# Kernel tuning notes

Hardware: AMD Instinct MI355X
Metric: run time of the kernel (lower is better)

Reference implementation:

```python
import jax, jax.numpy as jnp
import numpy as np

N_NODES = 100_000
N_EDGES = 800_000
NODE_DIM = 192
CONF_DIM = 64
HID = 256  # graphsage_in == graphsage_hidden
ALPHA = 0.2  # LeakyReLU negative slope


def _lrelu(x):
    return jnp.where(x >= 0, x, ALPHA * x)


def _sage_max(x, src, dst, wl, bl, wr):
    # PyG SAGEConv, aggr='max': out = lin_l(max_{j in N(i)} x_j) + lin_r(x_i)
    msgs = x[src]                                   # [E, HID] gather
    agg = jax.ops.segment_max(msgs, dst, num_segments=N_NODES)  # [N, HID]
    agg = jnp.where(jnp.isneginf(agg), 0.0, agg)    # isolated nodes -> 0
    return agg @ wl + bl + x @ wr


def _mlp2(x, w0, b0, w1, b1):
    # Linear -> LeakyReLU(0.2) -> Linear (activation only between layers)
    return _lrelu(x @ w0 + b0) @ w1 + b1


def setup_inputs() -> dict:
    key = jax.random.key(0)
    ks = jax.random.split(key, 16)
    s = 0.05
    inp = {
        "node_features": jax.random.normal(ks[0], (N_NODES, NODE_DIM), jnp.float32),
        "config_features": jax.random.normal(ks[1], (N_NODES, CONF_DIM), jnp.float32),
        "edges": jax.random.randint(ks[2], (2, N_EDGES), 0, N_NODES, jnp.int32),
        "prenet_w0": jax.random.normal(ks[3], (HID, NODE_DIM), jnp.float32) * s,
        "prenet_b0": jnp.zeros((NODE_DIM,), jnp.float32),
        "prenet_w1": jax.random.normal(ks[4], (NODE_DIM, NODE_DIM), jnp.float32) * s,
        "prenet_b1": jnp.zeros((NODE_DIM,), jnp.float32),
    }
    for l, k0 in ((0, 5), (1, 10)):
        inp[f"sage{l}_wl"] = jax.random.normal(ks[k0], (HID, HID), jnp.float32) * s
        inp[f"sage{l}_bl"] = jnp.zeros((HID,), jnp.float32)
        inp[f"sage{l}_wr"] = jax.random.normal(ks[k0 + 1], (HID, HID), jnp.float32) * s
        inp[f"mlp{l}_w0"] = jax.random.normal(ks[k0 + 2], (HID, NODE_DIM), jnp.float32) * s
        inp[f"mlp{l}_b0"] = jnp.zeros((NODE_DIM,), jnp.float32)
        inp[f"mlp{l}_w1"] = jax.random.normal(ks[k0 + 3], (NODE_DIM, NODE_DIM), jnp.float32) * s
        inp[f"mlp{l}_b1"] = jnp.zeros((NODE_DIM,), jnp.float32)
    return inp


def reference(node_features, config_features, edges,
              prenet_w0, prenet_b0, prenet_w1, prenet_b1,
              sage0_wl, sage0_bl, sage0_wr, mlp0_w0, mlp0_b0, mlp0_w1, mlp0_b1,
              sage1_wl, sage1_bl, sage1_wr, mlp1_w0, mlp1_b0, mlp1_w1, mlp1_b1):
    src, dst = edges[0], edges[1]
    x = jnp.concatenate([config_features, node_features], axis=1)  # [N, 256]
    x = _lrelu(_mlp2(x, prenet_w0, prenet_b0, prenet_w1, prenet_b1))  # [N, 192]
    layers = [
        (sage0_wl, sage0_bl, sage0_wr, mlp0_w0, mlp0_b0, mlp0_w1, mlp0_b1),
        (sage1_wl, sage1_bl, sage1_wr, mlp1_w0, mlp1_b0, mlp1_w1, mlp1_b1),
    ]
    for swl, sbl, swr, mw0, mb0, mw1, mb1 in layers:
        y = jnp.concatenate([config_features, x], axis=1)          # [N, 256]
        y = _sage_max(y, src, dst, swl, sbl, swr)                  # [N, 256]
        y = _lrelu(_mlp2(y, mw0, mb0, mw1, mb1))                   # [N, 192]
        x = x + y
    return x
```

## Files before the change

### kernel.cpp

```cpp
#include <hip/hip_runtime.h>
#include <stdint.h>

#define N_NODES 100000
#define N_EDGES 800000

typedef unsigned short u16;
typedef __attribute__((ext_vector_type(8))) short bf16x8;
typedef __attribute__((ext_vector_type(8))) unsigned short ushort8;
typedef __attribute__((ext_vector_type(4))) float f32x4;
typedef __attribute__((ext_vector_type(4))) int i32x4;
typedef __attribute__((ext_vector_type(4))) unsigned int u32x4;

struct alignas(8) U16x4 { u16 x, y, z, w; };

__device__ __forceinline__ u16 f2b(float f) {
    union { float f; unsigned u; } x; x.f = f;
    unsigned r = (x.u + 0x7FFFu + ((x.u >> 16) & 1u)) >> 16;
    return (u16)r;
}
__device__ __forceinline__ float b2f(u16 h) {
    union { unsigned u; float f; } x; x.u = ((unsigned)h) << 16;
    return x.f;
}
__device__ __forceinline__ u16 keyb(u16 h) {
    u16 m = (u16)((short)h >> 15);
    return (u16)(h ^ (0x8000u | (m & 0x7FFFu)));
}
__device__ __forceinline__ u16 unkey(u16 k) {
    u16 m = (u16)((short)k >> 15);
    return (u16)(k ^ (0x8000u | (~m & 0x7FFFu)));
}
__device__ __forceinline__ unsigned pkmax(unsigned a, unsigned b) {
    unsigned d;
    asm("v_pk_max_u16 %0, %1, %2" : "=v"(d) : "v"(a), "v"(b));
    return d;
}
__device__ __forceinline__ u32x4 pkmax4(u32x4 a, u32x4 b) {
    u32x4 r;
    r.x = pkmax(a.x, b.x); r.y = pkmax(a.y, b.y);
    r.z = pkmax(a.z, b.z); r.w = pkmax(a.w, b.w);
    return r;
}

__device__ __forceinline__ void gload_lds16(const void* g, void* l) {
    __builtin_amdgcn_global_load_lds(
        (const __attribute__((address_space(1))) char*)(uintptr_t)g,
        (__attribute__((address_space(3))) char*)(uintptr_t)l,
        16, 0, 0);
}

__device__ __forceinline__ int simgG(int row, int col) { return row * 136 + col; }
__device__ __forceinline__ int simgF(int row, int col) { return row * 200 + col; }


struct PackSeg { const float* a; const float* b; u16* dst; int K0, K1, Ncol, beg, end; };
struct PackArgs { PackSeg s[8]; };


__global__ void k_prep(const float* __restrict__ conf, const float* __restrict__ node,
                       u16* __restrict__ conf16, u16* __restrict__ node16,
                       u16* __restrict__ keyed, int* __restrict__ deg,
                       PackArgs p, int packTotal) {
    const int c4 = N_NODES * 64 / 4;
    const int n4 = N_NODES * 192 / 4;
    int i = blockIdx.x * blockDim.x + threadIdx.x;
    if (i < c4) {
        float4 v = ((const float4*)conf)[i];
        U16x4 o; o.x = f2b(v.x); o.y = f2b(v.y); o.z = f2b(v.z); o.w = f2b(v.w);
        ((U16x4*)conf16)[i] = o;
        U16x4 ko; ko.x = keyb(o.x); ko.y = keyb(o.y); ko.z = keyb(o.z); ko.w = keyb(o.w);
        int n = i >> 4;
        ((U16x4*)keyed)[n * 64 + (i & 15)] = ko;
    } else if (i < c4 + n4) {
        float4 v = ((const float4*)node)[i - c4];
        U16x4 o; o.x = f2b(v.x); o.y = f2b(v.y); o.z = f2b(v.z); o.w = f2b(v.w);
        ((U16x4*)node16)[i - c4] = o;
    } else if (i < c4 + n4 + N_NODES / 4) {
        i32x4 z = {0, 0, 0, 0};
        ((i32x4*)deg)[i - c4 - n4] = z;
    } else {
        int idx = i - (c4 + n4 + N_NODES / 4);
        if (idx < packTotal) {
            #pragma unroll
            for (int si = 0; si < 8; ++si) {
                if (idx >= p.s[si].beg && idx < p.s[si].end) {
                    int li = idx - p.s[si].beg;
                    int Ncol = p.s[si].Ncol, K0 = p.s[si].K0;
                    int kq = li & 7;
                    int t = li >> 3;
                    int c15 = t & 15; t >>= 4;
                    int k8 = t & 3;  t >>= 2;
                    int nb = Ncol >> 4;
                    int cb = t % nb;
                    int ks = t / nb;
                    int col = cb * 16 + c15;
                    int k = ks * 32 + k8 * 8 + kq;
                    float v = (k < K0) ? p.s[si].a[(size_t)k * Ncol + col]
                                       : p.s[si].b[(size_t)(k - K0) * Ncol + col];
                    p.s[si].dst[li] = f2b(v);
                }
            }
        }
    }
}


__global__ void k_count(const int* __restrict__ dst, int* __restrict__ deg) {
    int e = blockIdx.x * blockDim.x + threadIdx.x;
    if (e < N_EDGES) atomicAdd(&deg[dst[e]], 1);
}

__global__ void k_scan1(const int* __restrict__ deg, int* __restrict__ excl,
                        int* __restrict__ bsum, int n) {
    __shared__ int sh[512];
    int t = threadIdx.x;
    int base = blockIdx.x * 2048 + t * 4;
    int v0 = (base + 0 < n) ? deg[base + 0] : 0;
    int v1 = (base + 1 < n) ? deg[base + 1] : 0;
    int v2 = (base + 2 < n) ? deg[base + 2] : 0;
    int v3 = (base + 3 < n) ? deg[base + 3] : 0;
    int tot = v0 + v1 + v2 + v3;
    sh[t] = tot;
    __syncthreads();
    for (int off = 1; off < 512; off <<= 1) {
        int x = (t >= off) ? sh[t - off] : 0;
        __syncthreads();
        sh[t] += x;
        __syncthreads();
    }
    int run = sh[t] - tot;
    if (base + 0 < n) excl[base + 0] = run; run += v0;
    if (base + 1 < n) excl[base + 1] = run; run += v1;
    if (base + 2 < n) excl[base + 2] = run; run += v2;
    if (base + 3 < n) excl[base + 3] = run;
    if (t == 511) bsum[blockIdx.x] = sh[t];
}

__global__ void k_scan2(int* __restrict__ bsum, int nb) {
    __shared__ int sh[64];
    int t = threadIdx.x;
    int v = (t < nb) ? bsum[t] : 0;
    sh[t] = v;
    __syncthreads();
    for (int off = 1; off < 64; off <<= 1) {
        int x = (t >= off) ? sh[t - off] : 0;
        __syncthreads();
        sh[t] += x;
        __syncthreads();
    }
    if (t < nb) bsum[t] = sh[t] - v;
}

__global__ void k_scan3(int* __restrict__ excl, const int* __restrict__ bsum,
                        int* __restrict__ cursor, int n) {
    int i = blockIdx.x * blockDim.x + threadIdx.x;
    if (i < n) {
        int v = excl[i] + bsum[i >> 11];
        excl[i] = v;
        cursor[i] = v;
    }
}

__global__ void k_scatter(const int* __restrict__ src, const int* __restrict__ dst,
                          int* __restrict__ cursor, int* __restrict__ esrc) {
    int e = blockIdx.x * blockDim.x + threadIdx.x;
    if (e < N_EDGES) {
        int p = atomicAdd(&cursor[dst[e]], 1);
        esrc[p] = src[e];
    }
}


template<int CHUNKS>
__global__ __launch_bounds__(256) void k_agg(
    const u16* __restrict__ keyed,
    const int* __restrict__ indptr, const int* __restrict__ deg,
    const int* __restrict__ iend, const int* __restrict__ esrc,
    u16* __restrict__ agg, u16* __restrict__ aggC, int nquads) {
    __shared__ int se[512];
    __shared__ int sinfo[2];
    const int lane = threadIdx.x & 63;
    constexpr int ACTIVE = (CHUNKS == 32) ? 64 : 48;
    const int e_sub = (CHUNKS == 32) ? (lane >> 5) : (lane >= 24 ? 1 : 0);
    int ch = lane - e_sub * CHUNKS;
    if (ch < 0 || ch >= CHUNKS) ch = 0;
    const u16* bp = keyed + ((CHUNKS == 32) ? 0 : 64) + ch * 8;

    for (int q = blockIdx.x; q < nquads; q += gridDim.x) {
        const int b4 = q * 4;
        if (threadIdx.x == 0) {
            sinfo[0] = indptr[b4];
            sinfo[1] = iend[b4 + 3];
        }
        __syncthreads();
        const int sbase = sinfo[0];
        const int slen = sinfo[1] - sbase;
        const bool useLds = slen <= 512;
        if (useLds) {
            for (int i = threadIdx.x; i < slen; i += 256) se[i] = esrc[sbase + i];
        }
        __syncthreads();

        const int node = b4 + (threadIdx.x >> 6);
        const int start = indptr[node];
        const int d = deg[node];

        u32x4 m = {0u, 0u, 0u, 0u};

        if (lane < ACTIVE && d > 0) {
            const int rounds = (d + 15) >> 4;
            const int lbase = start - sbase;
            const int dm1 = d - 1;
            for (int rr = 0; rr < rounds; ++rr) {
                const int b0 = rr * 16 + e_sub;
                int s[8];
                if (useLds) {
                    #pragma unroll
                    for (int t = 0; t < 8; ++t) s[t] = se[lbase + min(b0 + 2 * t, dm1)];
                } else {
                    #pragma unroll
                    for (int t = 0; t < 8; ++t) s[t] = esrc[start + min(b0 + 2 * t, dm1)];
                }
                u32x4 v0 = *(const u32x4*)(bp + (size_t)s[0] * 256);
                u32x4 v1 = *(const u32x4*)(bp + (size_t)s[1] * 256);
                u32x4 v2 = *(const u32x4*)(bp + (size_t)s[2] * 256);
                u32x4 v3 = *(const u32x4*)(bp + (size_t)s[3] * 256);
                u32x4 v4 = *(const u32x4*)(bp + (size_t)s[4] * 256);
                u32x4 v5 = *(const u32x4*)(bp + (size_t)s[5] * 256);
                u32x4 v6 = *(const u32x4*)(bp + (size_t)s[6] * 256);
                u32x4 v7 = *(const u32x4*)(bp + (size_t)s[7] * 256);
                u32x4 a = pkmax4(pkmax4(v0, v1), pkmax4(v2, v3));
                u32x4 b = pkmax4(pkmax4(v4, v5), pkmax4(v6, v7));
                m = pkmax4(m, pkmax4(a, b));
            }
        }

        if (CHUNKS == 32) {
            m.x = pkmax(m.x, __shfl_xor(m.x, 32, 64));
            m.y = pkmax(m.y, __shfl_xor(m.y, 32, 64));
            m.z = pkmax(m.z, __shfl_xor(m.z, 32, 64));
            m.w = pkmax(m.w, __shfl_xor(m.w, 32, 64));
        } else {
            m.x = pkmax(m.x, __shfl(m.x, lane + 24, 64));
            m.y = pkmax(m.y, __shfl(m.y, lane + 24, 64));
            m.z = pkmax(m.z, __shfl(m.z, lane + 24, 64));
            m.w = pkmax(m.w, __shfl(m.w, lane + 24, 64));
        }

        unsigned wv[4] = {m.x, m.y, m.z, m.w};
        ushort8 o;
        #pragma unroll
        for (int j = 0; j < 4; ++j) {
            u16 klo = (u16)(wv[j] & 0xFFFFu), khi = (u16)(wv[j] >> 16);
            o[2 * j]     = (d > 0) ? unkey(klo) : (u16)0;
            o[2 * j + 1] = (d > 0) ? unkey(khi) : (u16)0;
        }

        if (CHUNKS == 32) {
            if (lane < 32) {
                *(ushort8*)(agg + (size_t)node * 256 + lane * 8) = o;
                if (lane < 8)
                    *(ushort8*)(aggC + (size_t)node * 64 + lane * 8) = o;
            }
        } else {
            if (lane < 24)
                *(ushort8*)(agg + (size_t)node * 256 + 64 + lane * 8) = o;
        }
        __syncthreads();
    }
}


struct SegA { const u16* p; int K; int stride; };

template<int BN>
__global__ __launch_bounds__(512) void k_gemm(
    SegA s0, SegA s1, SegA s2, SegA s3,
    const u16* __restrict__ Bt,
    const float* __restrict__ bias,
    u16* __restrict__ outb,
    int nrows)
{
    constexpr int FN = BN / 64;
    constexpr int ASZ = 128 * 32;
    __shared__ u16 lds[2][ASZ + BN * 32] __attribute__((aligned(16)));

    const int tid = threadIdx.x;
    const int wave = tid >> 6;
    const int lane = tid & 63;
    const int wr = wave >> 2;
    const int wc = wave & 3;
    const int rowbase = blockIdx.x * 128;
    const u16* segp[4] = {s0.p, s1.p, s2.p, s3.p};
    const int segK[4]  = {s0.K, s1.K, s2.K, s3.K};
    const int segS[4]  = {s0.stride, s1.stride, s2.stride, s3.stride};
    const int nk = (segK[0] + segK[1] + segK[2] + segK[3]) >> 5;

    const int arow = ((tid >> 6) << 4) | (tid & 15);
    int grow = rowbase + arow; if (grow >= nrows) grow = nrows - 1;
    const int ak8 = (tid >> 4) & 3;
    int seg = 0;
    const u16* gA = segp[0] + (size_t)grow * segS[0] + ak8 * 8;
    int segleft = segK[0] >> 5;
    const u16* gB0 = Bt + (size_t)tid * 8;
    const u16* gB1 = Bt + (size_t)(512 + tid) * 8;
    const int wb = wave * 512;

    auto adv = [&]() {
        gA += 32;
        if (--segleft == 0) {
            while (seg < 3) {
                ++seg;
                if (segK[seg] > 0) {
                    gA = segp[seg] + (size_t)grow * segS[seg] + ak8 * 8;
                    segleft = segK[seg] >> 5;
                    break;
                }
            }
        }
        gB0 += BN * 32;
        gB1 += BN * 32;
    };
    auto stage = [&](int buf) {
        gload_lds16(gA, &lds[buf][wb]);
        gload_lds16(gB0, &lds[buf][ASZ + wb]);
        if constexpr (BN == 256) {
            gload_lds16(gB1, &lds[buf][ASZ + 4096 + wb]);
        } else {
            if (tid < 256) gload_lds16(gB1, &lds[buf][ASZ + 4096 + wb]);
        }
    };

    f32x4 zero = {0.f, 0.f, 0.f, 0.f};
    f32x4 acc[4][FN];
    #pragma unroll
    for (int fm = 0; fm < 4; ++fm)
        #pragma unroll
        for (int fn = 0; fn < FN; ++fn)
            acc[fm][fn] = zero;

    stage(0); adv();
    __syncthreads();

    const int l15 = lane & 15, l4 = lane >> 4;

    for (int ks = 0; ks < nk; ++ks) {
        const int cur = ks & 1;
        if (ks + 1 < nk) { stage(cur ^ 1); adv(); }
        const u16* la = &lds[cur][0];
        const u16* lb = &lds[cur][ASZ];
        bf16x8 a[4], b[FN];
        #pragma unroll
        for (int fm = 0; fm < 4; ++fm)
            a[fm] = *(const bf16x8*)(la + (wr * 4 + fm) * 512 + lane * 8);
        #pragma unroll
        for (int fn = 0; fn < FN; ++fn)
            b[fn] = *(const bf16x8*)(lb + (wc * FN + fn) * 512 + lane * 8);
        #pragma unroll
        for (int fm = 0; fm < 4; ++fm)
            #pragma unroll
            for (int fn = 0; fn < FN; ++fn)
                acc[fm][fn] = __builtin_amdgcn_mfma_f32_16x16x32_bf16(a[fm], b[fn], acc[fm][fn], 0, 0, 0);
        __syncthreads();
    }

    u16* sbuf = &lds[0][0];
    #pragma unroll
    for (int chunk = 0; chunk < 2; ++chunk) {
        if ((wc >> 1) == chunk) {
            const int cbase = (wc & 1) * 64;
            #pragma unroll
            for (int fn = 0; fn < FN; ++fn) {
                const int cp = cbase + fn * 16 + l15;
                const float bs = bias[chunk * 128 + cp];
                #pragma unroll
                for (int fm = 0; fm < 4; ++fm) {
                    const int rbase = wr * 64 + fm * 16 + l4 * 4;
                    #pragma unroll
                    for (int r = 0; r < 4; ++r)
                        sbuf[simgG(rbase + r, cp)] = f2b(acc[fm][fn][r] + bs);
                }
            }
        }
        __syncthreads();
        #pragma unroll
        for (int j = 0; j < 4; ++j) {
            const int chk = j * 512 + tid;
            const int row = chk >> 4;
            const int cp = (chk & 15) * 8;
            const int gr = rowbase + row;
            if (gr < nrows) {
                ushort8 hv = *(const ushort8*)&sbuf[simgG(row, cp)];
                *(ushort8*)(outb + (size_t)gr * 256 + chunk * 128 + cp) = hv;
            }
        }
        __syncthreads();
    }
}


template<int EPI>
__global__ __launch_bounds__(512) void k_fused(
    const u16* __restrict__ A0, int K0,
    const u16* __restrict__ A1, int K1,
    const u16* __restrict__ B1t, const float* __restrict__ bias1,
    const u16* __restrict__ B2t, const float* __restrict__ bias2,
    float* __restrict__ outf, u16* __restrict__ outb,
    const u16* __restrict__ resid16, u16* __restrict__ keyed,
    int nrows)
{
    __shared__ u16 lds[25592] __attribute__((aligned(16)));

    const int tid = threadIdx.x;
    const int wave = tid >> 6;
    const int lane = tid & 63;
    const int wr = wave >> 2;
    const int wc = wave & 3;
    const int l15 = lane & 15, l4 = lane >> 4;
    const int rowbase = blockIdx.x * 128;
    const int nk1 = (K0 + K1) >> 5;

    const int arow = ((tid >> 6) << 4) | (tid & 15);
    int grow = rowbase + arow; if (grow >= nrows) grow = nrows - 1;
    const int ak8 = (tid >> 4) & 3;
    const u16* gA = A0 + (size_t)grow * K0 + ak8 * 8;
    int segleft = K0 >> 5;
    const u16* gB0 = B1t + (size_t)tid * 8;
    const u16* gB1 = B1t + (size_t)(512 + tid) * 8;
    const int wb = wave * 512;

    auto adv = [&]() {
        gA += 32;
        if (--segleft == 0 && K1 > 0) {
            gA = A1 + (size_t)grow * K1 + ak8 * 8;
            segleft = K1 >> 5;
        }
        gB0 += 6144;
        gB1 += 6144;
    };
    auto stage = [&](int buf) {
        gload_lds16(gA, &lds[buf * 4096 + wb]);
        gload_lds16(gB0, &lds[8192 + buf * 6144 + wb]);
        if (tid < 256) gload_lds16(gB1, &lds[8192 + buf * 6144 + 4096 + wb]);
    };

    f32x4 zero = {0.f, 0.f, 0.f, 0.f};
    f32x4 acc[4][3];
    #pragma unroll
    for (int fm = 0; fm < 4; ++fm)
        #pragma unroll
        for (int fn = 0; fn < 3; ++fn)
            acc[fm][fn] = zero;

    stage(0); adv();
    __syncthreads();

    for (int ks = 0; ks < nk1; ++ks) {
        const int cur = ks & 1;
        if (ks + 1 < nk1) { stage(cur ^ 1); adv(); }
        const u16* la = &lds[cur * 4096];
        const u16* lb = &lds[8192 + cur * 6144];
        bf16x8 a[4], b[3];
        #pragma unroll
        for (int fm = 0; fm < 4; ++fm)
            a[fm] = *(const bf16x8*)(la + (wr * 4 + fm) * 512 + lane * 8);
        #pragma unroll
        for (int fn = 0; fn < 3; ++fn)
            b[fn] = *(const bf16x8*)(lb + (wc * 3 + fn) * 512 + lane * 8);
        #pragma unroll
        for (int fm = 0; fm < 4; ++fm)
            #pragma unroll
            for (int fn = 0; fn < 3; ++fn)
                acc[fm][fn] = __builtin_amdgcn_mfma_f32_16x16x32_bf16(a[fm], b[fn], acc[fm][fn], 0, 0, 0);
        __syncthreads();
    }

    {
        const int c0 = wc * 48;
        #pragma unroll
        for (int fn = 0; fn < 3; ++fn) {
            const int c = c0 + fn * 16 + l15;
            const float bs = bias1[c];
            const int coff = (c >> 5) * 4096 + ((c >> 3) & 3) * 128 + (c & 7);
            #pragma unroll
            for (int fm = 0; fm < 4; ++fm) {
                const int rb = wr * 4 + fm;
                #pragma unroll
                for (int rr = 0; rr < 4; ++rr) {
                    const int r16 = l4 * 4 + rr;
                    float v = acc[fm][fn][rr] + bs;
                    v = (v >= 0.f) ? v : 0.2f * v;
                    lds[coff + rb * 512 + r16 * 8] = f2b(v);
                }
            }
        }
    }
    __syncthreads();

    bf16x8 breg[18];
    #pragma unroll
    for (int ks = 0; ks < 6; ++ks)
        #pragma unroll
        for (int fn = 0; fn < 3; ++fn)
            breg[ks * 3 + fn] = *(const bf16x8*)(B2t + (size_t)(ks * 12 + wc * 3 + fn) * 512 + lane * 8);

    f32x4 acc2[4][3];
    #pragma unroll
    for (int fm = 0; fm < 4; ++fm)
        #pragma unroll
        for (int fn = 0; fn < 3; ++fn)
            acc2[fm][fn] = zero;

    #pragma unroll
    for (int ks = 0; ks < 6; ++ks) {
        bf16x8 a2[4];
        #pragma unroll
        for (int fm = 0; fm < 4; ++fm)
            a2[fm] = *(const bf16x8*)(&lds[ks * 4096 + (wr * 4 + fm) * 512 + lane * 8]);
        #pragma unroll
        for (int fm = 0; fm < 4; ++fm)
            #pragma unroll
            for (int fn = 0; fn < 3; ++fn)
                acc2[fm][fn] = __builtin_amdgcn_mfma_f32_16x16x32_bf16(a2[fm], breg[ks * 3 + fn], acc2[fm][fn], 0, 0, 0);
    }
    __syncthreads();

    {
        const int c0 = wc * 48;
        #pragma unroll
        for (int fn = 0; fn < 3; ++fn) {
            const int c = c0 + fn * 16 + l15;
            const float bs = bias2[c];
            #pragma unroll
            for (int fm = 0; fm < 4; ++fm) {
                const int rbase = wr * 64 + fm * 16 + l4 * 4;
                #pragma unroll
                for (int r = 0; r < 4; ++r) {
                    float v = acc2[fm][fn][r] + bs;
                    v = (v >= 0.f) ? v : 0.2f * v;
                    lds[simgF(rbase + r, c)] = f2b(v);
                }
            }
        }
    }
    __syncthreads();

    #pragma unroll
    for (int j = 0; j < 6; ++j) {
        const int chk = j * 512 + tid;
        const int row = chk / 24;
        const int c = (chk - row * 24) * 8;
        const int gr = rowbase + row;
        if (gr < nrows) {
            ushort8 hv = *(const ushort8*)&lds[simgF(row, c)];
            if (EPI == 4) {
                ushort8 rv = *(const ushort8*)(resid16 + (size_t)gr * 192 + c);
                f32x4 o0, o1;
                #pragma unroll
                for (int k = 0; k < 4; ++k) {
                    o0[k] = b2f(hv[k]) + b2f(rv[k]);
                    o1[k] = b2f(hv[k + 4]) + b2f(rv[k + 4]);
                }
                *(f32x4*)(outf + (size_t)gr * 192 + c) = o0;
                *(f32x4*)(outf + (size_t)gr * 192 + c + 4) = o1;
            } else if (EPI == 5) {
                *(ushort8*)(outb + (size_t)gr * 192 + c) = hv;
                ushort8 kv;
                #pragma unroll
                for (int k = 0; k < 8; ++k) kv[k] = keyb(hv[k]);
                *(ushort8*)(keyed + (size_t)gr * 256 + 64 + c) = kv;
            } else {
                ushort8 rv = *(const ushort8*)(resid16 + (size_t)gr * 192 + c);
                ushort8 nb, kv;
                #pragma unroll
                for (int k = 0; k < 8; ++k) {
                    u16 hb = f2b(b2f(hv[k]) + b2f(rv[k]));
                    nb[k] = hb;
                    kv[k] = keyb(hb);
                }
                *(ushort8*)(outb + (size_t)gr * 192 + c) = nb;
                *(ushort8*)(keyed + (size_t)gr * 256 + 64 + c) = kv;
            }
        }
    }
}


extern "C" void kernel_launch(void* const* d_in, const int* in_sizes, int n_in,
                              void* d_out, int out_size, void* d_ws, size_t ws_size,
                              hipStream_t stream)
{
    (void)in_sizes; (void)n_in; (void)out_size; (void)ws_size;
    const float* node = (const float*)d_in[0];
    const float* conf = (const float*)d_in[1];
    const int* edges  = (const int*)d_in[2];
    const float* pw0  = (const float*)d_in[3];
    const float* pb0  = (const float*)d_in[4];
    const float* pw1  = (const float*)d_in[5];
    const float* pb1  = (const float*)d_in[6];
    const float* W[14];
    for (int i = 0; i < 14; ++i) W[i] = (const float*)d_in[7 + i];
    float* out = (float*)d_out;
    const int* e_src = edges;
    const int* e_dst = edges + N_EDGES;

    u16* keyed = (u16*)d_out;

    char* w = (char*)d_ws;
    auto alloc = [&](size_t b) { char* p = w; w += (b + 255) & ~(size_t)255; return p; };
    u16* conf16 = (u16*)alloc((size_t)N_NODES * 64 * 2);
    u16* node16 = (u16*)alloc((size_t)N_NODES * 192 * 2);
    u16* x16    = (u16*)alloc((size_t)N_NODES * 192 * 2);
    u16* agg16  = (u16*)alloc((size_t)N_NODES * 256 * 2);
    u16* aggC   = (u16*)alloc((size_t)N_NODES * 64 * 2);
    int* deg    = (int*)alloc((size_t)N_NODES * 4);
    int* indptr = (int*)alloc((size_t)N_NODES * 4);
    int* cursor = (int*)alloc((size_t)N_NODES * 4);
    int* esrc   = (int*)alloc((size_t)N_EDGES * 4);
    int* bsum   = (int*)alloc(4096);
    u16* pw0t   = (u16*)alloc((size_t)192 * 256 * 2);
    u16* pw1t   = (u16*)alloc((size_t)192 * 192 * 2);
    u16 *sB[2], *mw0t[2], *mw1t[2];
    for (int l = 0; l < 2; ++l) {
        sB[l]   = (u16*)alloc((size_t)256 * 512 * 2);
        mw0t[l] = (u16*)alloc((size_t)192 * 256 * 2);
        mw1t[l] = (u16*)alloc((size_t)192 * 192 * 2);
    }

    {
        PackArgs pa;
        int off = 0;
        auto seg = [&](int i, const float* a, int K0, const float* b, int K1, int Ncol, u16* dst) {
            int sz = Ncol * (K0 + K1);
            pa.s[i] = {a, b, dst, K0, K1, Ncol, off, off + sz};
            off += sz;
        };
        seg(0, pw0, 256, nullptr, 0, 192, pw0t);
        seg(1, pw1, 192, nullptr, 0, 192, pw1t);
        seg(2, W[0], 256, W[2], 256, 256, sB[0]);
        seg(3, W[3], 256, nullptr, 0, 192, mw0t[0]);
        seg(4, W[5], 192, nullptr, 0, 192, mw1t[0]);
        seg(5, W[7], 256, W[9], 256, 256, sB[1]);
        seg(6, W[10], 256, nullptr, 0, 192, mw0t[1]);
        seg(7, W[12], 192, nullptr, 0, 192, mw1t[1]);
        const int tot = N_NODES * 64 / 4 + N_NODES * 192 / 4 + N_NODES / 4 + off;
        k_prep<<<(tot + 255) / 256, 256, 0, stream>>>(conf, node, conf16, node16,
                                                      keyed, deg, pa, off);
    }
    k_count<<<(N_EDGES + 255) / 256, 256, 0, stream>>>(e_dst, deg);
    int nb = (N_NODES + 2047) / 2048;
    k_scan1<<<nb, 512, 0, stream>>>(deg, indptr, bsum, N_NODES);
    k_scan2<<<1, 64, 0, stream>>>(bsum, nb);
    k_scan3<<<(N_NODES + 255) / 256, 256, 0, stream>>>(indptr, bsum, cursor, N_NODES);
    k_scatter<<<(N_EDGES + 255) / 256, 256, 0, stream>>>(e_src, e_dst, cursor, esrc);

    const int gblk = (N_NODES + 127) / 128;
    const int nquads = N_NODES / 4;
    k_fused<5><<<gblk, 512, 0, stream>>>(conf16, 64, node16, 192,
                                         pw0t, pb0, pw1t, pb1,
                                         nullptr, x16, nullptr, keyed, N_NODES);
    for (int l = 0; l < 2; ++l) {
        if (l == 0) {
            k_agg<32><<<2048, 256, 0, stream>>>(keyed, indptr, deg, cursor, esrc,
                                                agg16, aggC, nquads);
            k_gemm<256><<<gblk, 512, 0, stream>>>(
                SegA{agg16, 256, 256}, SegA{conf16, 64, 64},
                SegA{x16, 192, 192}, SegA{nullptr, 0, 0},
                sB[0], W[1], agg16, N_NODES);
        } else {
            k_agg<24><<<2048, 256, 0, stream>>>(keyed, indptr, deg, cursor, esrc,
                                                agg16, aggC, nquads);
            k_gemm<256><<<gblk, 512, 0, stream>>>(
                SegA{aggC, 64, 64}, SegA{agg16 + 64, 192, 256},
                SegA{conf16, 64, 64}, SegA{x16, 192, 192},
                sB[1], W[8], agg16, N_NODES);
        }
        if (l == 0)
            k_fused<6><<<gblk, 512, 0, stream>>>(agg16, 256, nullptr, 0,
                                                 mw0t[0], W[4], mw1t[0], W[6],
                                                 nullptr, x16, x16, keyed, N_NODES);
        else
            k_fused<4><<<gblk, 512, 0, stream>>>(agg16, 256, nullptr, 0,
                                                 mw0t[1], W[11], mw1t[1], W[13],
                                                 out, nullptr, x16, nullptr, N_NODES);
    }
}
```

Baseline: 446.0 us.

## Split keyed gather buffer into dense conf and x arrays, one quad per block

The interleaved 256-wide keyed buffer is split into a 64-wide conf array and a 192-wide x array with dense strides. The layer-1 gather, which reads only the x part, now touches contiguous 384-byte rows instead of strided 512-byte rows, which improves cache-line use. The aggregation kernel also drops its grid-stride loop and launches one block per 4-node quad, removing the per-iteration barriers at the cost of more, shorter-lived blocks. keyedC is placed after keyedX inside the output buffer, which relies on that buffer being large enough.

```diff
diff --git a/kernel.cpp b/kernel.cpp
--- a/kernel.cpp
+++ b/kernel.cpp
@@ -59,7 +59,7 @@
 
 __global__ void k_prep(const float* __restrict__ conf, const float* __restrict__ node,
                        u16* __restrict__ conf16, u16* __restrict__ node16,
-                       u16* __restrict__ keyed, int* __restrict__ deg,
+                       u16* __restrict__ keyedC, int* __restrict__ deg,
                        PackArgs p, int packTotal) {
     const int c4 = N_NODES * 64 / 4;
     const int n4 = N_NODES * 192 / 4;
@@ -69,8 +69,7 @@
         U16x4 o; o.x = f2b(v.x); o.y = f2b(v.y); o.z = f2b(v.z); o.w = f2b(v.w);
         ((U16x4*)conf16)[i] = o;
         U16x4 ko; ko.x = keyb(o.x); ko.y = keyb(o.y); ko.z = keyb(o.z); ko.w = keyb(o.w);
-        int n = i >> 4;
-        ((U16x4*)keyed)[n * 64 + (i & 15)] = ko;
+        ((U16x4*)keyedC)[i] = ko;
     } else if (i < c4 + n4) {
         float4 v = ((const float4*)node)[i - c4];
         U16x4 o; o.x = f2b(v.x); o.y = f2b(v.y); o.z = f2b(v.z); o.w = f2b(v.w);
@@ -173,100 +172,106 @@
 
 template<int CHUNKS>
 __global__ __launch_bounds__(256) void k_agg(
-    const u16* __restrict__ keyed,
+    const u16* __restrict__ keyedC, const u16* __restrict__ keyedX,
     const int* __restrict__ indptr, const int* __restrict__ deg,
     const int* __restrict__ iend, const int* __restrict__ esrc,
-    u16* __restrict__ agg, u16* __restrict__ aggC, int nquads) {
+    u16* __restrict__ agg, u16* __restrict__ aggC) {
     __shared__ int se[512];
     __shared__ int sinfo[2];
+    const int b4 = blockIdx.x * 4;
+    if (threadIdx.x == 0) {
+        sinfo[0] = indptr[b4];
+        sinfo[1] = iend[b4 + 3];
+    }
+    __syncthreads();
+    const int sbase = sinfo[0];
+    const int slen = sinfo[1] - sbase;
+    const bool useLds = slen <= 512;
+    if (useLds) {
+        for (int i = threadIdx.x; i < slen; i += 256) se[i] = esrc[sbase + i];
+    }
+    __syncthreads();
+
+    const int node = b4 + (threadIdx.x >> 6);
     const int lane = threadIdx.x & 63;
     constexpr int ACTIVE = (CHUNKS == 32) ? 64 : 48;
     const int e_sub = (CHUNKS == 32) ? (lane >> 5) : (lane >= 24 ? 1 : 0);
     int ch = lane - e_sub * CHUNKS;
     if (ch < 0 || ch >= CHUNKS) ch = 0;
-    const u16* bp = keyed + ((CHUNKS == 32) ? 0 : 64) + ch * 8;
-
-    for (int q = blockIdx.x; q < nquads; q += gridDim.x) {
-        const int b4 = q * 4;
-        if (threadIdx.x == 0) {
-            sinfo[0] = indptr[b4];
-            sinfo[1] = iend[b4 + 3];
-        }
-        __syncthreads();
-        const int sbase = sinfo[0];
-        const int slen = sinfo[1] - sbase;
-        const bool useLds = slen <= 512;
-        if (useLds) {
-            for (int i = threadIdx.x; i < slen; i += 256) se[i] = esrc[sbase + i];
-        }
-        __syncthreads();
-
-        const int node = b4 + (threadIdx.x >> 6);
-        const int start = indptr[node];
-        const int d = deg[node];
-
-        u32x4 m = {0u, 0u, 0u, 0u};
-
-        if (lane < ACTIVE && d > 0) {
-            const int rounds = (d + 15) >> 4;
-            const int lbase = start - sbase;
-            const int dm1 = d - 1;
-            for (int rr = 0; rr < rounds; ++rr) {
-                const int b0 = rr * 16 + e_sub;
-                int s[8];
-                if (useLds) {
-                    #pragma unroll
-                    for (int t = 0; t < 8; ++t) s[t] = se[lbase + min(b0 + 2 * t, dm1)];
-                } else {
-                    #pragma unroll
-                    for (int t = 0; t < 8; ++t) s[t] = esrc[start + min(b0 + 2 * t, dm1)];
-                }
-                u32x4 v0 = *(const u32x4*)(bp + (size_t)s[0] * 256);
-                u32x4 v1 = *(const u32x4*)(bp + (size_t)s[1] * 256);
-                u32x4 v2 = *(const u32x4*)(bp + (size_t)s[2] * 256);
-                u32x4 v3 = *(const u32x4*)(bp + (size_t)s[3] * 256);
-                u32x4 v4 = *(const u32x4*)(bp + (size_t)s[4] * 256);
-                u32x4 v5 = *(const u32x4*)(bp + (size_t)s[5] * 256);
-                u32x4 v6 = *(const u32x4*)(bp + (size_t)s[6] * 256);
-                u32x4 v7 = *(const u32x4*)(bp + (size_t)s[7] * 256);
-                u32x4 a = pkmax4(pkmax4(v0, v1), pkmax4(v2, v3));
-                u32x4 b = pkmax4(pkmax4(v4, v5), pkmax4(v6, v7));
-                m = pkmax4(m, pkmax4(a, b));
-            }
-        }
-
-        if (CHUNKS == 32) {
-            m.x = pkmax(m.x, __shfl_xor(m.x, 32, 64));
-            m.y = pkmax(m.y, __shfl_xor(m.y, 32, 64));
-            m.z = pkmax(m.z, __shfl_xor(m.z, 32, 64));
-            m.w = pkmax(m.w, __shfl_xor(m.w, 32, 64));
-        } else {
-            m.x = pkmax(m.x, __shfl(m.x, lane + 24, 64));
-            m.y = pkmax(m.y, __shfl(m.y, lane + 24, 64));
-            m.z = pkmax(m.z, __shfl(m.z, lane + 24, 64));
-            m.w = pkmax(m.w, __shfl(m.w, lane + 24, 64));
-        }
-
-        unsigned wv[4] = {m.x, m.y, m.z, m.w};
-        ushort8 o;
-        #pragma unroll
-        for (int j = 0; j < 4; ++j) {
-            u16 klo = (u16)(wv[j] & 0xFFFFu), khi = (u16)(wv[j] >> 16);
-            o[2 * j]     = (d > 0) ? unkey(klo) : (u16)0;
-            o[2 * j + 1] = (d > 0) ? unkey(khi) : (u16)0;
-        }
-
-        if (CHUNKS == 32) {
-            if (lane < 32) {
-                *(ushort8*)(agg + (size_t)node * 256 + lane * 8) = o;
-                if (lane < 8)
-                    *(ushort8*)(aggC + (size_t)node * 64 + lane * 8) = o;
-            }
-        } else {
-            if (lane < 24)
-                *(ushort8*)(agg + (size_t)node * 256 + 64 + lane * 8) = o;
-        }
-        __syncthreads();
+    const int start = indptr[node];
+    const int d = deg[node];
+
+    const u16* bp;
+    int stride;
+    if (CHUNKS == 32) {
+        const bool isConf = ch < 8;
+        bp = isConf ? (keyedC + ch * 8) : (keyedX + (ch - 8) * 8);
+        stride = isConf ? 64 : 192;
+    } else {
+        bp = keyedX + ch * 8;
+        stride = 192;
+    }
+
+    u32x4 m = {0u, 0u, 0u, 0u};
+
+    if (lane < ACTIVE && d > 0) {
+        const int rounds = (d + 15) >> 4;
+        const int lbase = start - sbase;
+        const int dm1 = d - 1;
+        for (int rr = 0; rr < rounds; ++rr) {
+            const int b0 = rr * 16 + e_sub;
+            int s[8];
+            if (useLds) {
+                #pragma unroll
+                for (int t = 0; t < 8; ++t) s[t] = se[lbase + min(b0 + 2 * t, dm1)];
+            } else {
+                #pragma unroll
+                for (int t = 0; t < 8; ++t) s[t] = esrc[start + min(b0 + 2 * t, dm1)];
+            }
+            u32x4 v0 = *(const u32x4*)(bp + (size_t)s[0] * stride);
+            u32x4 v1 = *(const u32x4*)(bp + (size_t)s[1] * stride);
+            u32x4 v2 = *(const u32x4*)(bp + (size_t)s[2] * stride);
+            u32x4 v3 = *(const u32x4*)(bp + (size_t)s[3] * stride);
+            u32x4 v4 = *(const u32x4*)(bp + (size_t)s[4] * stride);
+            u32x4 v5 = *(const u32x4*)(bp + (size_t)s[5] * stride);
+            u32x4 v6 = *(const u32x4*)(bp + (size_t)s[6] * stride);
+            u32x4 v7 = *(const u32x4*)(bp + (size_t)s[7] * stride);
+            u32x4 a = pkmax4(pkmax4(v0, v1), pkmax4(v2, v3));
+            u32x4 b = pkmax4(pkmax4(v4, v5), pkmax4(v6, v7));
+            m = pkmax4(m, pkmax4(a, b));
+        }
+    }
+
+    if (CHUNKS == 32) {
+        m.x = pkmax(m.x, __shfl_xor(m.x, 32, 64));
+        m.y = pkmax(m.y, __shfl_xor(m.y, 32, 64));
+        m.z = pkmax(m.z, __shfl_xor(m.z, 32, 64));
+        m.w = pkmax(m.w, __shfl_xor(m.w, 32, 64));
+    } else {
+        m.x = pkmax(m.x, __shfl(m.x, lane + 24, 64));
+        m.y = pkmax(m.y, __shfl(m.y, lane + 24, 64));
+        m.z = pkmax(m.z, __shfl(m.z, lane + 24, 64));
+        m.w = pkmax(m.w, __shfl(m.w, lane + 24, 64));
+    }
+
+    unsigned wv[4] = {m.x, m.y, m.z, m.w};
+    ushort8 o;
+    #pragma unroll
+    for (int j = 0; j < 4; ++j) {
+        u16 klo = (u16)(wv[j] & 0xFFFFu), khi = (u16)(wv[j] >> 16);
+        o[2 * j]     = (d > 0) ? unkey(klo) : (u16)0;
+        o[2 * j + 1] = (d > 0) ? unkey(khi) : (u16)0;
+    }
+
+    if (CHUNKS == 32) {
+        if (lane < 32) {
+            *(ushort8*)(agg + (size_t)node * 256 + lane * 8) = o;
+            if (lane < 8)
+                *(ushort8*)(aggC + (size_t)node * 64 + lane * 8) = o;
+        }
+    } else {
+        if (lane < 24)
+            *(ushort8*)(agg + (size_t)node * 256 + 64 + lane * 8) = o;
     }
 }
 
@@ -406,7 +411,7 @@
     const u16* __restrict__ B1t, const float* __restrict__ bias1,
     const u16* __restrict__ B2t, const float* __restrict__ bias2,
     float* __restrict__ outf, u16* __restrict__ outb,
-    const u16* __restrict__ resid16, u16* __restrict__ keyed,
+    const u16* __restrict__ resid16, u16* __restrict__ keyedX,
     int nrows)
 {
     __shared__ u16 lds[25592] __attribute__((aligned(16)));
@@ -568,7 +573,7 @@
                 ushort8 kv;
                 #pragma unroll
                 for (int k = 0; k < 8; ++k) kv[k] = keyb(hv[k]);
-                *(ushort8*)(keyed + (size_t)gr * 256 + 64 + c) = kv;
+                *(ushort8*)(keyedX + (size_t)gr * 192 + c) = kv;
             } else {
                 ushort8 rv = *(const ushort8*)(resid16 + (size_t)gr * 192 + c);
                 ushort8 nb, kv;
@@ -579,7 +584,7 @@
                     kv[k] = keyb(hb);
                 }
                 *(ushort8*)(outb + (size_t)gr * 192 + c) = nb;
-                *(ushort8*)(keyed + (size_t)gr * 256 + 64 + c) = kv;
+                *(ushort8*)(keyedX + (size_t)gr * 192 + c) = kv;
             }
         }
     }
@@ -604,7 +609,8 @@
     const int* e_src = edges;
     const int* e_dst = edges + N_EDGES;
 
-    u16* keyed = (u16*)d_out;
+    u16* keyedX = (u16*)d_out;
+    u16* keyedC = (u16*)d_out + (size_t)N_NODES * 192;
 
     char* w = (char*)d_ws;
     auto alloc = [&](size_t b) { char* p = w; w += (b + 255) & ~(size_t)255; return p; };
@@ -645,7 +651,7 @@
         seg(7, W[12], 192, nullptr, 0, 192, mw1t[1]);
         const int tot = N_NODES * 64 / 4 + N_NODES * 192 / 4 + N_NODES / 4 + off;
         k_prep<<<(tot + 255) / 256, 256, 0, stream>>>(conf, node, conf16, node16,
-                                                      keyed, deg, pa, off);
+                                                      keyedC, deg, pa, off);
     }
     k_count<<<(N_EDGES + 255) / 256, 256, 0, stream>>>(e_dst, deg);
     int nb = (N_NODES + 2047) / 2048;
@@ -655,21 +661,20 @@
     k_scatter<<<(N_EDGES + 255) / 256, 256, 0, stream>>>(e_src, e_dst, cursor, esrc);
 
     const int gblk = (N_NODES + 127) / 128;
-    const int nquads = N_NODES / 4;
     k_fused<5><<<gblk, 512, 0, stream>>>(conf16, 64, node16, 192,
                                          pw0t, pb0, pw1t, pb1,
-                                         nullptr, x16, nullptr, keyed, N_NODES);
+                                         nullptr, x16, nullptr, keyedX, N_NODES);
     for (int l = 0; l < 2; ++l) {
         if (l == 0) {
-            k_agg<32><<<2048, 256, 0, stream>>>(keyed, indptr, deg, cursor, esrc,
-                                                agg16, aggC, nquads);
+            k_agg<32><<<N_NODES / 4, 256, 0, stream>>>(keyedC, keyedX, indptr, deg,
+                                                       cursor, esrc, agg16, aggC);
             k_gemm<256><<<gblk, 512, 0, stream>>>(
                 SegA{agg16, 256, 256}, SegA{conf16, 64, 64},
                 SegA{x16, 192, 192}, SegA{nullptr, 0, 0},
                 sB[0], W[1], agg16, N_NODES);
         } else {
-            k_agg<24><<<2048, 256, 0, stream>>>(keyed, indptr, deg, cursor, esrc,
-                                                agg16, aggC, nquads);
+            k_agg<24><<<N_NODES / 4, 256, 0, stream>>>(keyedC, keyedX, indptr, deg,
+                                                       cursor, esrc, agg16, aggC);
             k_gemm<256><<<gblk, 512, 0, stream>>>(
                 SegA{aggC, 64, 64}, SegA{agg16 + 64, 192, 256},
                 SegA{conf16, 64, 64}, SegA{x16, 192, 192},
@@ -678,7 +683,7 @@
         if (l == 0)
             k_fused<6><<<gblk, 512, 0, stream>>>(agg16, 256, nullptr, 0,
                                                  mw0t[0], W[4], mw1t[0], W[6],
-                                                 nullptr, x16, x16, keyed, N_NODES);
+                                                 nullptr, x16, x16, keyedX, N_NODES);
         else
             k_fused<4><<<gblk, 512, 0, stream>>>(agg16, 256, nullptr, 0,
                                                  mw0t[1], W[11], mw1t[1], W[13],
```

Measured after the change: 445.1 us. About the same (-0.2%).
